# Kernel optimization log

Measured on AMD Instinct MI355X. Metric: run time of the kernel, lower is better.

## Reference

```python
import jax, jax.numpy as jnp
import numpy as np

D_MODEL = 1024
N_HEADS = 16
HEAD_DIM = D_MODEL // N_HEADS
SEQ_LEN = 2048
BATCH = 2
ROPE_THETA = 10000.0
EPS = 1e-8
SCALE = 1.0 / np.sqrt(HEAD_DIM)
MASK_VAL = -10000.0  # module uses -10000.0, not -inf


def _rope_tables(seq_len, head_dim, theta):
    inv = 1.0 / (theta ** (jnp.arange(0, head_dim, 2, dtype=jnp.float32) / head_dim))
    ang = jnp.arange(seq_len, dtype=jnp.float32)[:, None] * inv[None, :]  # [S, hd/2]
    return jnp.cos(ang), jnp.sin(ang)


def _apply_rope(t, cos, sin):
    # t: [B,S,H,hd]; pairs are consecutive elements (torch.view_as_complex layout)
    B, S, H, hd = t.shape
    tr = t.reshape(B, S, H, hd // 2, 2)
    te, to = tr[..., 0], tr[..., 1]
    c = cos[None, :, None, :]
    s = sin[None, :, None, :]
    out = jnp.stack([te * c - to * s, te * s + to * c], axis=-1)
    return out.reshape(B, S, H, hd)


def _rmsnorm(t, gamma):
    rms = jnp.sqrt(jnp.mean(t * t, axis=-1, keepdims=True) + EPS)
    return t / rms * gamma


def setup_inputs() -> dict:
    key = jax.random.key(0)
    ks = jax.random.split(key, 7)
    sw = 0.02  # weight scale ~ xavier
    return {
        "x": jax.random.normal(ks[0], (BATCH, SEQ_LEN, D_MODEL), jnp.float32),
        "wq": jax.random.normal(ks[1], (D_MODEL, D_MODEL), jnp.float32) * sw,
        "wk": jax.random.normal(ks[2], (D_MODEL, D_MODEL), jnp.float32) * sw,
        "wv": jax.random.normal(ks[3], (D_MODEL, D_MODEL), jnp.float32) * sw,
        "wo": jax.random.normal(ks[4], (D_MODEL, D_MODEL), jnp.float32) * sw,
        "q_gamma": jnp.ones((HEAD_DIM,), jnp.float32),
        "k_gamma": jnp.ones((HEAD_DIM,), jnp.float32),
    }


def reference(x, wq, wk, wv, wo, q_gamma, k_gamma):
    B, S, D = x.shape
    H, hd = N_HEADS, HEAD_DIM
    # projections (nn.Linear: y = x @ W.T)
    q = (x @ wq.T).reshape(B, S, H, hd)
    k = (x @ wk.T).reshape(B, S, H, hd)
    v = (x @ wv.T).reshape(B, S, H, hd)
    # RoPE
    cos, sin = _rope_tables(S, hd, ROPE_THETA)
    q = _apply_rope(q, cos, sin)
    k = _apply_rope(k, cos, sin)
    # QK RMSNorm
    q = _rmsnorm(q, q_gamma)
    k = _rmsnorm(k, k_gamma)
    # attention, causal mask with -10000.0 fill
    scores = jnp.einsum("bqhd,bkhd->bhqk", q, k) * SCALE
    causal = jnp.triu(jnp.ones((S, S), bool), k=1)
    scores = jnp.where(causal[None, None], MASK_VAL, scores)
    attn = jax.nn.softmax(scores, axis=-1)
    out = jnp.einsum("bhqk,bkhd->bqhd", attn, v).reshape(B, S, D)
    return out @ wo.T
```

## Files before the change

### kernel.cpp

```cpp
#include <hip/hip_runtime.h>
#include <hip/hip_bf16.h>
#include <stdint.h>

#define D_MODEL 1024
#define N_HEADS 16
#define HEAD_DIM 64
#define SEQ_LEN 2048
#define BATCH 2
#define M_TOK (BATCH * SEQ_LEN)
#define NQT (SEQ_LEN / 64)
#define SCL2 0.18033688011112042f
#define RMS_EPS 1e-8f

typedef __bf16 bf16x8 __attribute__((ext_vector_type(8)));
typedef float f32x4 __attribute__((ext_vector_type(4)));
typedef unsigned short us8 __attribute__((ext_vector_type(8)));
typedef unsigned short us4 __attribute__((ext_vector_type(4)));

__device__ __forceinline__ float bf2f(unsigned short u) {
    union { unsigned int i; float f; } x; x.i = ((unsigned int)u) << 16; return x.f;
}
__device__ __forceinline__ unsigned short f2bf(float f) {
    union { float f; unsigned int i; } x; x.f = f;
    unsigned int i = x.i;
    return (unsigned short)((i + 0x7FFFu + ((i >> 16) & 1u)) >> 16);
}
__device__ __forceinline__ f32x4 mfma16(bf16x8 a, bf16x8 b, f32x4 c) {
    return __builtin_amdgcn_mfma_f32_16x16x32_bf16(a, b, c, 0, 0, 0);
}

#define GLOAD16(gp, lp) __builtin_amdgcn_global_load_lds( \
    (__attribute__((address_space(1))) void*)(gp), \
    (__attribute__((address_space(3))) void*)(lp), 16, 0, 0)

__device__ __forceinline__ uint32_t lds_off(void* p) {
    return (uint32_t)(uintptr_t)(__attribute__((address_space(3))) char*)p;
}
__device__ __forceinline__ uint2 ds_tr16(uint32_t addr) {
    uint2 r;
    asm volatile("ds_read_b64_tr_b16 %0, %1" : "=v"(r) : "v"(addr));
    return r;
}

__global__ void f2bf_kernel(const float* __restrict__ in,
                            unsigned short* __restrict__ out, int n4) {
    int i = blockIdx.x * blockDim.x + threadIdx.x;
    if (i >= n4) return;
    float4 v = reinterpret_cast<const float4*>(in)[i];
    us4 o = { f2bf(v.x), f2bf(v.y), f2bf(v.z), f2bf(v.w) };
    reinterpret_cast<us4*>(out)[i] = o;
}

__global__ void f2bf_multi_kernel(const float* __restrict__ s0, const float* __restrict__ s1,
                                  const float* __restrict__ s2, const float* __restrict__ s3,
                                  unsigned short* __restrict__ d0, unsigned short* __restrict__ d1,
                                  unsigned short* __restrict__ d2, unsigned short* __restrict__ d3) {
    int i = blockIdx.x * 256 + threadIdx.x;
    int mm = i >> 18, j = i & 262143;
    const float* s = mm == 0 ? s0 : mm == 1 ? s1 : mm == 2 ? s2 : s3;
    unsigned short* d = mm == 0 ? d0 : mm == 1 ? d1 : mm == 2 ? d2 : d3;
    float4 v = reinterpret_cast<const float4*>(s)[j];
    us4 o = { f2bf(v.x), f2bf(v.y), f2bf(v.z), f2bf(v.w) };
    reinterpret_cast<us4*>(d)[j] = o;
}

__global__ void rope_tab_kernel(float2* __restrict__ tab) {
    int idx = blockIdx.x * 256 + threadIdx.x;
    int pos = idx >> 5, i = idx & 31;
    float inv = powf(10000.0f, -(float)(2 * i) / 64.0f);
    float ang = (float)pos * inv;
    tab[idx] = make_float2(cosf(ang), sinf(ang));
}

template <typename OutT, int NMAT>
__global__ __launch_bounds__(256, 2)
void gemm_bt_kernel(const unsigned short* __restrict__ A,
                    const unsigned short* __restrict__ B0,
                    const unsigned short* __restrict__ B1,
                    const unsigned short* __restrict__ B2,
                    OutT* __restrict__ C0, OutT* __restrict__ C1,
                    OutT* __restrict__ C2, int M, int N, int K) {
    __shared__ __align__(16) char lds[32768];
    char* Ab = lds;
    char* Bb = lds + 16384;

    const unsigned short* Bm = B0;
    OutT* Cm = C0;
    if (NMAT > 1) {
        int z = blockIdx.z;
        if (z == 1) { Bm = B1; Cm = C1; }
        else if (z == 2) { Bm = B2; Cm = C2; }
    }

    const int tid = threadIdx.x;
    const int w = tid >> 6, lane = tid & 63;
    const int g = lane >> 4, c15 = lane & 15;
    const int wr = w >> 1, wc = w & 1;
    const int m0 = blockIdx.y * 128, n0 = blockIdx.x * 128;
    const int row_s = tid >> 3, k8 = tid & 7;

    f32x4 acc[4][4] = {};
    const int NT = K >> 6;

    for (int kt = 0; kt < NT; ++kt) {
        const int kb = kt * 64;
        __syncthreads();
#pragma unroll
        for (int r = 0; r < 4; ++r) {
            int row = r * 32 + row_s;
            GLOAD16(A + (size_t)(m0 + row) * K + kb + k8 * 8, Ab + r * 4096 + w * 1024);
            GLOAD16(Bm + (size_t)(n0 + row) * K + kb + k8 * 8, Bb + r * 4096 + w * 1024);
        }
        __syncthreads();

        bf16x8 af[4][2], bfr[4][2];
#pragma unroll
        for (int mi = 0; mi < 4; ++mi)
#pragma unroll
            for (int kk = 0; kk < 2; ++kk) {
                af[mi][kk]  = *reinterpret_cast<const bf16x8*>(Ab + (wr * 64 + mi * 16 + c15) * 128 + kk * 64 + g * 16);
                bfr[mi][kk] = *reinterpret_cast<const bf16x8*>(Bb + (wc * 64 + mi * 16 + c15) * 128 + kk * 64 + g * 16);
            }
#pragma unroll
        for (int mi = 0; mi < 4; ++mi)
#pragma unroll
            for (int nj = 0; nj < 4; ++nj)
#pragma unroll
                for (int kk = 0; kk < 2; ++kk)
                    acc[mi][nj] = mfma16(af[mi][kk], bfr[nj][kk], acc[mi][nj]);
    }

#pragma unroll
    for (int mi = 0; mi < 4; ++mi)
#pragma unroll
        for (int nj = 0; nj < 4; ++nj)
#pragma unroll
            for (int r = 0; r < 4; ++r) {
                int row = m0 + wr * 64 + mi * 16 + g * 4 + r;
                int col = n0 + wc * 64 + nj * 16 + c15;
                float v = acc[mi][nj][r];
                if constexpr (sizeof(OutT) == 2)
                    Cm[(size_t)row * N + col] = f2bf(v);
                else
                    Cm[(size_t)row * N + col] = v;
            }
}

__global__ void rope_rms_kernel(unsigned short* __restrict__ Q,
                                unsigned short* __restrict__ Kt,
                                const float* __restrict__ qg,
                                const float* __restrict__ kg,
                                const float2* __restrict__ tab) {
    unsigned short* T = blockIdx.z ? Kt : Q;
    const float* gam = blockIdx.z ? kg : qg;
    int t = blockIdx.x * 256 + threadIdx.x;
    int rp = t >> 2, sub = t & 3;
    int s = (rp >> 4) & (SEQ_LEN - 1);
    unsigned short* p = T + (size_t)rp * 64 + sub * 16;
    float f[16];
    us8 v0 = *reinterpret_cast<const us8*>(p);
    us8 v1 = *reinterpret_cast<const us8*>(p + 8);
#pragma unroll
    for (int j = 0; j < 8; ++j) { f[j] = bf2f(v0[j]); f[8 + j] = bf2f(v1[j]); }
#pragma unroll
    for (int j = 0; j < 8; ++j) {
        float2 cs = tab[s * 32 + sub * 8 + j];
        float e = f[2 * j], o = f[2 * j + 1];
        f[2 * j]     = e * cs.x - o * cs.y;
        f[2 * j + 1] = e * cs.y + o * cs.x;
    }
    float ss = 0.f;
#pragma unroll
    for (int j = 0; j < 16; ++j) ss += f[j] * f[j];
    ss += __shfl_xor(ss, 1);
    ss += __shfl_xor(ss, 2);
    float rinv = rsqrtf(ss * (1.0f / 64.0f) + RMS_EPS);
    us8 o0, o1;
#pragma unroll
    for (int j = 0; j < 8; ++j) {
        o0[j] = f2bf(f[j] * rinv * gam[sub * 16 + j]);
        o1[j] = f2bf(f[8 + j] * rinv * gam[sub * 16 + 8 + j]);
    }
    *reinterpret_cast<us8*>(p) = o0;
    *reinterpret_cast<us8*>(p + 8) = o1;
}

__global__ __launch_bounds__(256, 2)
void attn_kernel(const unsigned short* __restrict__ Q,
                 const unsigned short* __restrict__ Kt,
                 const unsigned short* __restrict__ V,
                 unsigned short* __restrict__ O) {
    __shared__ __align__(16) char lds[40960];
    const int bh = blockIdx.y, b = bh >> 4, h = bh & 15;
    const int tid = threadIdx.x, w = tid >> 6, lane = tid & 63;
    const int g = lane >> 4, c15 = lane & 15;
    char* Pw = lds + 32768 + w * 2048;
    const size_t base_bh = (size_t)b * SEQ_LEN * D_MODEL + (size_t)h * HEAD_DIM;
    const int krow_s = tid >> 3, kcol_s = (tid & 7) * 16;
    const int psw = (c15 & 7) << 4;

    auto stageKV = [&](int buf, int kb) {
#pragma unroll
        for (int r = 0; r < 2; ++r) {
            int krow = r * 32 + krow_s;
            int cb = kcol_s ^ ((krow & 7) << 4);
            GLOAD16(Kt + base_bh + (size_t)(kb + krow) * D_MODEL + (cb >> 1),
                    lds + buf * 8192 + r * 4096 + w * 1024);
            int e = r * 2048 + tid * 8;
            int vk = ((e >> 8) << 2) + ((e >> 4) & 3);
            int vd = (((e >> 6) & 3) << 4) + (e & 15);
            GLOAD16(V + base_bh + (size_t)(kb + vk) * D_MODEL + vd,
                    lds + 16384 + buf * 8192 + r * 4096 + w * 1024);
        }
    };

#pragma unroll 1
    for (int half = 0; half < 2; ++half) {
        const int qt = half ? (NQT - 1 - blockIdx.x) : blockIdx.x;
        const int q0 = qt * 64, nt = qt + 1;
        const int q = q0 + w * 16 + c15;
        bf16x8 qf[2];
#pragma unroll
        for (int kk = 0; kk < 2; ++kk)
            qf[kk] = *reinterpret_cast<const bf16x8*>(Q + base_bh + (size_t)q * D_MODEL + kk * 32 + g * 8);
        f32x4 oacc[4] = {};
        float mrun = -1e30f, lrun = 0.f;

        stageKV(0, 0);
        __syncthreads();
        for (int it = 0; it < nt; ++it) {
            const int cur = it & 1, kb = it * 64;
            if (it + 1 < nt) stageKV(cur ^ 1, kb + 64);
            char* Kc = lds + cur * 8192;
            char* Vc = lds + 16384 + cur * 8192;

            f32x4 sacc[4] = {};
#pragma unroll
            for (int nj = 0; nj < 4; ++nj) {
                int kl = nj * 16 + c15, sw = (kl & 7) << 4;
#pragma unroll
                for (int kk = 0; kk < 2; ++kk) {
                    bf16x8 kf = *reinterpret_cast<const bf16x8*>(Kc + kl * 128 + ((kk * 64 + g * 16) ^ sw));
                    sacc[nj] = mfma16(kf, qf[kk], sacc[nj]);
                }
            }

            const bool diag = (it == nt - 1);
            float sv[4][4];
            float tmax = -1e30f;
#pragma unroll
            for (int nj = 0; nj < 4; ++nj)
#pragma unroll
                for (int r = 0; r < 4; ++r) {
                    float s = sacc[nj][r] * SCL2;
                    if (diag && (kb + nj * 16 + g * 4 + r > q)) s = -1e30f;
                    sv[nj][r] = s;
                    tmax = fmaxf(tmax, s);
                }
            tmax = fmaxf(tmax, __shfl_xor(tmax, 16));
            tmax = fmaxf(tmax, __shfl_xor(tmax, 32));
            float mnew = fmaxf(mrun, tmax);
            float alpha = exp2f(mrun - mnew);
            float rsum = 0.f;
#pragma unroll
            for (int nj = 0; nj < 4; ++nj) {
                us4 pw;
#pragma unroll
                for (int r = 0; r < 4; ++r) {
                    float p = exp2f(sv[nj][r] - mnew);
                    rsum += p;
                    pw[r] = f2bf(p);
                }
                *reinterpret_cast<us4*>(Pw + c15 * 128 + ((nj * 32 + g * 8) ^ psw)) = pw;
            }
            rsum += __shfl_xor(rsum, 16);
            rsum += __shfl_xor(rsum, 32);
            lrun = lrun * alpha + rsum;
            mrun = mnew;

            float ar[4];
#pragma unroll
            for (int r = 0; r < 4; ++r) ar[r] = __shfl(alpha, g * 4 + r, 16);
#pragma unroll
            for (int f = 0; f < 4; ++f)
#pragma unroll
                for (int r = 0; r < 4; ++r) oacc[f][r] *= ar[r];

            bf16x8 pf[2];
#pragma unroll
            for (int kk = 0; kk < 2; ++kk)
                pf[kk] = *reinterpret_cast<const bf16x8*>(Pw + c15 * 128 + ((kk * 64 + g * 16) ^ psw));
            uint32_t vbase = lds_off(Vc) + c15 * 8;
            uint2 vt[4][2][2];
#pragma unroll
            for (int f = 0; f < 4; ++f)
#pragma unroll
                for (int kk = 0; kk < 2; ++kk)
#pragma unroll
                    for (int hh = 0; hh < 2; ++hh)
                        vt[f][kk][hh] = ds_tr16(vbase + (uint32_t)((kk * 8 + g * 2 + hh) * 512 + f * 128));
            asm volatile("s_waitcnt lgkmcnt(0)" ::: "memory");
            __builtin_amdgcn_sched_barrier(0);
#pragma unroll
            for (int f = 0; f < 4; ++f)
#pragma unroll
                for (int kk = 0; kk < 2; ++kk) {
                    union { uint32_t u[4]; bf16x8 v; } fu;
                    fu.u[0] = vt[f][kk][0].x; fu.u[1] = vt[f][kk][0].y;
                    fu.u[2] = vt[f][kk][1].x; fu.u[3] = vt[f][kk][1].y;
                    oacc[f] = mfma16(pf[kk], fu.v, oacc[f]);
                }
            __syncthreads();
        }

        float li = 1.f / lrun;
        float lr[4];
#pragma unroll
        for (int r = 0; r < 4; ++r) lr[r] = __shfl(li, g * 4 + r, 16);
#pragma unroll
        for (int f = 0; f < 4; ++f)
#pragma unroll
            for (int r = 0; r < 4; ++r) {
                int qq = q0 + w * 16 + g * 4 + r;
                O[base_bh + (size_t)qq * D_MODEL + f * 16 + c15] = f2bf(oacc[f][r] * lr[r]);
            }
    }
}

extern "C" void kernel_launch(void* const* d_in, const int* in_sizes, int n_in,
                              void* d_out, int out_size, void* d_ws, size_t ws_size,
                              hipStream_t stream) {
    const float* x  = (const float*)d_in[0];
    const float* wq = (const float*)d_in[1];
    const float* wk = (const float*)d_in[2];
    const float* wv = (const float*)d_in[3];
    const float* wo = (const float*)d_in[4];
    const float* qg = (const float*)d_in[5];
    const float* kg = (const float*)d_in[6];
    float* out = (float*)d_out;

    char* ws = (char*)d_ws;
    const size_t MB = 1024ull * 1024ull;
    unsigned short* xb  = (unsigned short*)(ws);
    unsigned short* qb  = (unsigned short*)(ws + 8 * MB);
    unsigned short* kb  = (unsigned short*)(ws + 16 * MB);
    unsigned short* vb  = (unsigned short*)(ws + 24 * MB);
    unsigned short* ab  = (unsigned short*)(ws + 32 * MB);
    unsigned short* wqb = (unsigned short*)(ws + 40 * MB);
    unsigned short* wkb = (unsigned short*)(ws + 42 * MB);
    unsigned short* wvb = (unsigned short*)(ws + 44 * MB);
    unsigned short* wob = (unsigned short*)(ws + 46 * MB);
    float2* tab         = (float2*)(ws + 48 * MB);

    f2bf_kernel<<<4096, 256, 0, stream>>>(x, xb, M_TOK * D_MODEL / 4);
    f2bf_multi_kernel<<<4096, 256, 0, stream>>>(wq, wk, wv, wo, wqb, wkb, wvb, wob);
    rope_tab_kernel<<<256, 256, 0, stream>>>(tab);

    gemm_bt_kernel<unsigned short, 3><<<dim3(8, 32, 3), 256, 0, stream>>>(
        xb, wqb, wkb, wvb, qb, kb, vb, M_TOK, D_MODEL, D_MODEL);

    rope_rms_kernel<<<dim3(1024, 1, 2), 256, 0, stream>>>(qb, kb, qg, kg, tab);

    attn_kernel<<<dim3(16, 32), 256, 0, stream>>>(qb, kb, vb, ab);

    gemm_bt_kernel<float, 1><<<dim3(8, 32, 1), 256, 0, stream>>>(
        ab, wob, nullptr, nullptr, out, nullptr, nullptr, M_TOK, D_MODEL, D_MODEL);
}
```

Baseline: 215.0 us.

## Fuse prep kernels, fold RoPE+RMSNorm into QKV GEMM epilogue, defer softmax rescale

Merges the three conversion and RoPE-table kernels into one prep launch. RoPE and RMSNorm, including the softmax scale for Q, move into the QKV GEMM epilogue, which removes the separate read-modify-write pass over Q and K. The attention loop skips the running-max rescale unless the max rises by more than a threshold, packs bf16 with v_cvt_pk_bf16_f32, and raises wave priority around the MFMA blocks. The output projection uses 64-row tiles so more blocks run, and the epilogue adds shuffles and table loads inside the GEMM.

```diff
diff --git a/kernel.cpp b/kernel.cpp
--- a/kernel.cpp
+++ b/kernel.cpp
@@ -11,6 +11,7 @@
 #define NQT (SEQ_LEN / 64)
 #define SCL2 0.18033688011112042f
 #define RMS_EPS 1e-8f
+#define DEFER_THR 11.5f
 
 typedef __bf16 bf16x8 __attribute__((ext_vector_type(8)));
 typedef float f32x4 __attribute__((ext_vector_type(4)));
@@ -28,6 +29,11 @@
 __device__ __forceinline__ f32x4 mfma16(bf16x8 a, bf16x8 b, f32x4 c) {
     return __builtin_amdgcn_mfma_f32_16x16x32_bf16(a, b, c, 0, 0, 0);
 }
+__device__ __forceinline__ uint32_t cvtpk_bf16(float lo, float hi) {
+    uint32_t r;
+    asm("v_cvt_pk_bf16_f32 %0, %1, %2" : "=v"(r) : "v"(lo), "v"(hi));
+    return r;
+}
 
 #define GLOAD16(gp, lp) __builtin_amdgcn_global_load_lds( \
     (__attribute__((address_space(1))) void*)(gp), \
@@ -42,61 +48,61 @@
     return r;
 }
 
-__global__ void f2bf_kernel(const float* __restrict__ in,
-                            unsigned short* __restrict__ out, int n4) {
-    int i = blockIdx.x * blockDim.x + threadIdx.x;
-    if (i >= n4) return;
-    float4 v = reinterpret_cast<const float4*>(in)[i];
-    us4 o = { f2bf(v.x), f2bf(v.y), f2bf(v.z), f2bf(v.w) };
-    reinterpret_cast<us4*>(out)[i] = o;
-}
-
-__global__ void f2bf_multi_kernel(const float* __restrict__ s0, const float* __restrict__ s1,
-                                  const float* __restrict__ s2, const float* __restrict__ s3,
-                                  unsigned short* __restrict__ d0, unsigned short* __restrict__ d1,
-                                  unsigned short* __restrict__ d2, unsigned short* __restrict__ d3) {
-    int i = blockIdx.x * 256 + threadIdx.x;
-    int mm = i >> 18, j = i & 262143;
-    const float* s = mm == 0 ? s0 : mm == 1 ? s1 : mm == 2 ? s2 : s3;
-    unsigned short* d = mm == 0 ? d0 : mm == 1 ? d1 : mm == 2 ? d2 : d3;
-    float4 v = reinterpret_cast<const float4*>(s)[j];
-    us4 o = { f2bf(v.x), f2bf(v.y), f2bf(v.z), f2bf(v.w) };
-    reinterpret_cast<us4*>(d)[j] = o;
-}
-
-__global__ void rope_tab_kernel(float2* __restrict__ tab) {
-    int idx = blockIdx.x * 256 + threadIdx.x;
-    int pos = idx >> 5, i = idx & 31;
-    float inv = powf(10000.0f, -(float)(2 * i) / 64.0f);
-    float ang = (float)pos * inv;
-    tab[idx] = make_float2(cosf(ang), sinf(ang));
-}
-
-template <typename OutT, int NMAT>
+__global__ void prep_kernel(const float* __restrict__ x,  const float* __restrict__ wq,
+                            const float* __restrict__ wk, const float* __restrict__ wv,
+                            const float* __restrict__ wo,
+                            unsigned short* __restrict__ xb,  unsigned short* __restrict__ wqb,
+                            unsigned short* __restrict__ wkb, unsigned short* __restrict__ wvb,
+                            unsigned short* __restrict__ wob, float2* __restrict__ tab2) {
+    int bid = blockIdx.x;
+    if (bid < 8192) {
+        int i = bid * 256 + threadIdx.x;
+        const float* s; unsigned short* d; int j;
+        if (i < 1048576) { s = x; d = xb; j = i; }
+        else {
+            int t = i - 1048576; int mm = t >> 18; j = t & 262143;
+            s = mm == 0 ? wq : mm == 1 ? wk : mm == 2 ? wv : wo;
+            d = mm == 0 ? wqb : mm == 1 ? wkb : mm == 2 ? wvb : wob;
+        }
+        float4 v = reinterpret_cast<const float4*>(s)[j];
+        us4 o = { f2bf(v.x), f2bf(v.y), f2bf(v.z), f2bf(v.w) };
+        reinterpret_cast<us4*>(d)[j] = o;
+    } else {
+        int idx = (bid - 8192) * 256 + threadIdx.x;
+        int i = idx >> 11, sp = idx & 2047;
+        float inv = powf(10000.0f, -(float)(2 * i) / 64.0f);
+        float ang = (float)sp * inv;
+        tab2[idx] = make_float2(cosf(ang), sinf(ang));
+    }
+}
+
 __global__ __launch_bounds__(256, 2)
-void gemm_bt_kernel(const unsigned short* __restrict__ A,
-                    const unsigned short* __restrict__ B0,
-                    const unsigned short* __restrict__ B1,
-                    const unsigned short* __restrict__ B2,
-                    OutT* __restrict__ C0, OutT* __restrict__ C1,
-                    OutT* __restrict__ C2, int M, int N, int K) {
+void gemm_qkv_kernel(const unsigned short* __restrict__ A,
+                     const unsigned short* __restrict__ Bq,
+                     const unsigned short* __restrict__ Bk,
+                     const unsigned short* __restrict__ Bv,
+                     unsigned short* __restrict__ Cq,
+                     unsigned short* __restrict__ Ck,
+                     unsigned short* __restrict__ Cv,
+                     const float* __restrict__ qg,
+                     const float* __restrict__ kg,
+                     const float2* __restrict__ tab2) {
+    const int K = D_MODEL, N = D_MODEL;
     __shared__ __align__(16) char lds[32768];
     char* Ab = lds;
     char* Bb = lds + 16384;
 
-    const unsigned short* Bm = B0;
-    OutT* Cm = C0;
-    if (NMAT > 1) {
-        int z = blockIdx.z;
-        if (z == 1) { Bm = B1; Cm = C1; }
-        else if (z == 2) { Bm = B2; Cm = C2; }
-    }
+    const int nb = blockIdx.x;
+    const int mtype = nb >> 3;
+    const int ncol = (nb & 7) * 128;
+    const unsigned short* Bm = mtype == 0 ? Bq : mtype == 1 ? Bk : Bv;
+    unsigned short* Cm = mtype == 0 ? Cq : mtype == 1 ? Ck : Cv;
 
     const int tid = threadIdx.x;
     const int w = tid >> 6, lane = tid & 63;
     const int g = lane >> 4, c15 = lane & 15;
     const int wr = w >> 1, wc = w & 1;
-    const int m0 = blockIdx.y * 128, n0 = blockIdx.x * 128;
+    const int m0 = blockIdx.y * 128;
     const int row_s = tid >> 3, k8 = tid & 7;
 
     f32x4 acc[4][4] = {};
@@ -109,7 +115,7 @@
         for (int r = 0; r < 4; ++r) {
             int row = r * 32 + row_s;
             GLOAD16(A + (size_t)(m0 + row) * K + kb + k8 * 8, Ab + r * 4096 + w * 1024);
-            GLOAD16(Bm + (size_t)(n0 + row) * K + kb + k8 * 8, Bb + r * 4096 + w * 1024);
+            GLOAD16(Bm + (size_t)(ncol + row) * K + kb + k8 * 8, Bb + r * 4096 + w * 1024);
         }
         __syncthreads();
 
@@ -130,59 +136,131 @@
                     acc[mi][nj] = mfma16(af[mi][kk], bfr[nj][kk], acc[mi][nj]);
     }
 
-#pragma unroll
-    for (int mi = 0; mi < 4; ++mi)
+    if (mtype == 2) {
+#pragma unroll
+        for (int mi = 0; mi < 4; ++mi)
+#pragma unroll
+            for (int nj = 0; nj < 4; ++nj)
+#pragma unroll
+                for (int r = 0; r < 4; ++r) {
+                    int row = m0 + wr * 64 + mi * 16 + g * 4 + r;
+                    int col = ncol + wc * 64 + nj * 16 + c15;
+                    Cm[(size_t)row * N + col] = f2bf(acc[mi][nj][r]);
+                }
+        return;
+    }
+
+    const float* gam = mtype ? kg : qg;
+    const float qsc = mtype ? 1.0f : SCL2;
+    float g4[4];
+#pragma unroll
+    for (int nj = 0; nj < 4; ++nj) g4[nj] = gam[nj * 16 + c15] * qsc;
+    const int ihalf = c15 >> 1;
+
+#pragma unroll
+    for (int mi = 0; mi < 4; ++mi) {
+        int rbase = m0 + wr * 64 + mi * 16 + g * 4;
+        int srow = rbase & (SEQ_LEN - 1);
+        float2 cs[4][4];
+#pragma unroll
+        for (int nj = 0; nj < 4; ++nj) {
+            const float4* tp = reinterpret_cast<const float4*>(tab2 + (size_t)(nj * 8 + ihalf) * SEQ_LEN + srow);
+            float4 lo = tp[0], hi = tp[1];
+            cs[nj][0] = make_float2(lo.x, lo.y); cs[nj][1] = make_float2(lo.z, lo.w);
+            cs[nj][2] = make_float2(hi.x, hi.y); cs[nj][3] = make_float2(hi.z, hi.w);
+        }
+        float rot[4][4];
 #pragma unroll
         for (int nj = 0; nj < 4; ++nj)
 #pragma unroll
             for (int r = 0; r < 4; ++r) {
-                int row = m0 + wr * 64 + mi * 16 + g * 4 + r;
+                float v = acc[mi][nj][r];
+                float pv = __shfl_xor(v, 1);
+                float c = cs[nj][r].x, s = cs[nj][r].y;
+                rot[nj][r] = (c15 & 1) ? fmaf(pv, s, v * c) : fmaf(-pv, s, v * c);
+            }
+#pragma unroll
+        for (int r = 0; r < 4; ++r) {
+            float ss = rot[0][r] * rot[0][r] + rot[1][r] * rot[1][r]
+                     + rot[2][r] * rot[2][r] + rot[3][r] * rot[3][r];
+            ss += __shfl_xor(ss, 1);
+            ss += __shfl_xor(ss, 2);
+            ss += __shfl_xor(ss, 4);
+            ss += __shfl_xor(ss, 8);
+            float rinv = rsqrtf(ss * (1.0f / 64.0f) + RMS_EPS);
+#pragma unroll
+            for (int nj = 0; nj < 4; ++nj) {
+                int col = ncol + wc * 64 + nj * 16 + c15;
+                Cm[(size_t)(rbase + r) * N + col] = f2bf(rot[nj][r] * rinv * g4[nj]);
+            }
+        }
+    }
+}
+
+__global__ __launch_bounds__(256, 2)
+void gemm_proj_kernel(const unsigned short* __restrict__ A,
+                      const unsigned short* __restrict__ B,
+                      float* __restrict__ C) {
+    const int K = D_MODEL, N = D_MODEL;
+    __shared__ __align__(16) char lds[24576];
+    char* Ab = lds;
+    char* Bb = lds + 8192;
+
+    const int tid = threadIdx.x;
+    const int w = tid >> 6, lane = tid & 63;
+    const int g = lane >> 4, c15 = lane & 15;
+    const int wr = w >> 1, wc = w & 1;
+    const int m0 = blockIdx.y * 64, n0 = blockIdx.x * 128;
+    const int row_s = tid >> 3, k8 = tid & 7;
+
+    f32x4 acc[2][4] = {};
+    const int NT = K >> 6;
+
+    for (int kt = 0; kt < NT; ++kt) {
+        const int kb = kt * 64;
+        __syncthreads();
+#pragma unroll
+        for (int r = 0; r < 2; ++r) {
+            int row = r * 32 + row_s;
+            GLOAD16(A + (size_t)(m0 + row) * K + kb + k8 * 8, Ab + r * 4096 + w * 1024);
+        }
+#pragma unroll
+        for (int r = 0; r < 4; ++r) {
+            int row = r * 32 + row_s;
+            GLOAD16(B + (size_t)(n0 + row) * K + kb + k8 * 8, Bb + r * 4096 + w * 1024);
+        }
+        __syncthreads();
+
+        bf16x8 af[2][2], bfr[4][2];
+#pragma unroll
+        for (int mi = 0; mi < 2; ++mi)
+#pragma unroll
+            for (int kk = 0; kk < 2; ++kk)
+                af[mi][kk] = *reinterpret_cast<const bf16x8*>(Ab + (wr * 32 + mi * 16 + c15) * 128 + kk * 64 + g * 16);
+#pragma unroll
+        for (int nj = 0; nj < 4; ++nj)
+#pragma unroll
+            for (int kk = 0; kk < 2; ++kk)
+                bfr[nj][kk] = *reinterpret_cast<const bf16x8*>(Bb + (wc * 64 + nj * 16 + c15) * 128 + kk * 64 + g * 16);
+#pragma unroll
+        for (int mi = 0; mi < 2; ++mi)
+#pragma unroll
+            for (int nj = 0; nj < 4; ++nj)
+#pragma unroll
+                for (int kk = 0; kk < 2; ++kk)
+                    acc[mi][nj] = mfma16(af[mi][kk], bfr[nj][kk], acc[mi][nj]);
+    }
+
+#pragma unroll
+    for (int mi = 0; mi < 2; ++mi)
+#pragma unroll
+        for (int nj = 0; nj < 4; ++nj)
+#pragma unroll
+            for (int r = 0; r < 4; ++r) {
+                int row = m0 + wr * 32 + mi * 16 + g * 4 + r;
                 int col = n0 + wc * 64 + nj * 16 + c15;
-                float v = acc[mi][nj][r];
-                if constexpr (sizeof(OutT) == 2)
-                    Cm[(size_t)row * N + col] = f2bf(v);
-                else
-                    Cm[(size_t)row * N + col] = v;
-            }
-}
-
-__global__ void rope_rms_kernel(unsigned short* __restrict__ Q,
-                                unsigned short* __restrict__ Kt,
-                                const float* __restrict__ qg,
-                                const float* __restrict__ kg,
-                                const float2* __restrict__ tab) {
-    unsigned short* T = blockIdx.z ? Kt : Q;
-    const float* gam = blockIdx.z ? kg : qg;
-    int t = blockIdx.x * 256 + threadIdx.x;
-    int rp = t >> 2, sub = t & 3;
-    int s = (rp >> 4) & (SEQ_LEN - 1);
-    unsigned short* p = T + (size_t)rp * 64 + sub * 16;
-    float f[16];
-    us8 v0 = *reinterpret_cast<const us8*>(p);
-    us8 v1 = *reinterpret_cast<const us8*>(p + 8);
-#pragma unroll
-    for (int j = 0; j < 8; ++j) { f[j] = bf2f(v0[j]); f[8 + j] = bf2f(v1[j]); }
-#pragma unroll
-    for (int j = 0; j < 8; ++j) {
-        float2 cs = tab[s * 32 + sub * 8 + j];
-        float e = f[2 * j], o = f[2 * j + 1];
-        f[2 * j]     = e * cs.x - o * cs.y;
-        f[2 * j + 1] = e * cs.y + o * cs.x;
-    }
-    float ss = 0.f;
-#pragma unroll
-    for (int j = 0; j < 16; ++j) ss += f[j] * f[j];
-    ss += __shfl_xor(ss, 1);
-    ss += __shfl_xor(ss, 2);
-    float rinv = rsqrtf(ss * (1.0f / 64.0f) + RMS_EPS);
-    us8 o0, o1;
-#pragma unroll
-    for (int j = 0; j < 8; ++j) {
-        o0[j] = f2bf(f[j] * rinv * gam[sub * 16 + j]);
-        o1[j] = f2bf(f[8 + j] * rinv * gam[sub * 16 + 8 + j]);
-    }
-    *reinterpret_cast<us8*>(p) = o0;
-    *reinterpret_cast<us8*>(p + 8) = o1;
+                C[(size_t)row * N + col] = acc[mi][nj][r];
+            }
 }
 
 __global__ __launch_bounds__(256, 2)
@@ -235,6 +313,7 @@
             char* Vc = lds + 16384 + cur * 8192;
 
             f32x4 sacc[4] = {};
+            __builtin_amdgcn_s_setprio(1);
 #pragma unroll
             for (int nj = 0; nj < 4; ++nj) {
                 int kl = nj * 16 + c15, sw = (kl & 7) << 4;
@@ -244,6 +323,7 @@
                     sacc[nj] = mfma16(kf, qf[kk], sacc[nj]);
                 }
             }
+            __builtin_amdgcn_s_setprio(0);
 
             const bool diag = (it == nt - 1);
             float sv[4][4];
@@ -252,39 +332,42 @@
             for (int nj = 0; nj < 4; ++nj)
 #pragma unroll
                 for (int r = 0; r < 4; ++r) {
-                    float s = sacc[nj][r] * SCL2;
+                    float s = sacc[nj][r];
                     if (diag && (kb + nj * 16 + g * 4 + r > q)) s = -1e30f;
                     sv[nj][r] = s;
                     tmax = fmaxf(tmax, s);
                 }
             tmax = fmaxf(tmax, __shfl_xor(tmax, 16));
             tmax = fmaxf(tmax, __shfl_xor(tmax, 32));
-            float mnew = fmaxf(mrun, tmax);
-            float alpha = exp2f(mrun - mnew);
+
+            float alpha = 1.0f;
+            if (__any(tmax > mrun + DEFER_THR)) {
+                float mnew = fmaxf(mrun, tmax);
+                alpha = exp2f(mrun - mnew);
+                mrun = mnew;
+                float ar[4];
+#pragma unroll
+                for (int r = 0; r < 4; ++r) ar[r] = __shfl(alpha, g * 4 + r, 16);
+#pragma unroll
+                for (int f = 0; f < 4; ++f)
+#pragma unroll
+                    for (int r = 0; r < 4; ++r) oacc[f][r] *= ar[r];
+            }
+
             float rsum = 0.f;
 #pragma unroll
             for (int nj = 0; nj < 4; ++nj) {
-                us4 pw;
-#pragma unroll
-                for (int r = 0; r < 4; ++r) {
-                    float p = exp2f(sv[nj][r] - mnew);
-                    rsum += p;
-                    pw[r] = f2bf(p);
-                }
-                *reinterpret_cast<us4*>(Pw + c15 * 128 + ((nj * 32 + g * 8) ^ psw)) = pw;
+                float p0 = exp2f(sv[nj][0] - mrun);
+                float p1 = exp2f(sv[nj][1] - mrun);
+                float p2 = exp2f(sv[nj][2] - mrun);
+                float p3 = exp2f(sv[nj][3] - mrun);
+                rsum += (p0 + p1) + (p2 + p3);
+                uint2 pw = { cvtpk_bf16(p0, p1), cvtpk_bf16(p2, p3) };
+                *reinterpret_cast<uint2*>(Pw + c15 * 128 + ((nj * 32 + g * 8) ^ psw)) = pw;
             }
             rsum += __shfl_xor(rsum, 16);
             rsum += __shfl_xor(rsum, 32);
             lrun = lrun * alpha + rsum;
-            mrun = mnew;
-
-            float ar[4];
-#pragma unroll
-            for (int r = 0; r < 4; ++r) ar[r] = __shfl(alpha, g * 4 + r, 16);
-#pragma unroll
-            for (int f = 0; f < 4; ++f)
-#pragma unroll
-                for (int r = 0; r < 4; ++r) oacc[f][r] *= ar[r];
 
             bf16x8 pf[2];
 #pragma unroll
@@ -301,6 +384,7 @@
                         vt[f][kk][hh] = ds_tr16(vbase + (uint32_t)((kk * 8 + g * 2 + hh) * 512 + f * 128));
             asm volatile("s_waitcnt lgkmcnt(0)" ::: "memory");
             __builtin_amdgcn_sched_barrier(0);
+            __builtin_amdgcn_s_setprio(1);
 #pragma unroll
             for (int f = 0; f < 4; ++f)
 #pragma unroll
@@ -310,6 +394,7 @@
                     fu.u[2] = vt[f][kk][1].x; fu.u[3] = vt[f][kk][1].y;
                     oacc[f] = mfma16(pf[kk], fu.v, oacc[f]);
                 }
+            __builtin_amdgcn_s_setprio(0);
             __syncthreads();
         }
 
@@ -350,19 +435,14 @@
     unsigned short* wkb = (unsigned short*)(ws + 42 * MB);
     unsigned short* wvb = (unsigned short*)(ws + 44 * MB);
     unsigned short* wob = (unsigned short*)(ws + 46 * MB);
-    float2* tab         = (float2*)(ws + 48 * MB);
-
-    f2bf_kernel<<<4096, 256, 0, stream>>>(x, xb, M_TOK * D_MODEL / 4);
-    f2bf_multi_kernel<<<4096, 256, 0, stream>>>(wq, wk, wv, wo, wqb, wkb, wvb, wob);
-    rope_tab_kernel<<<256, 256, 0, stream>>>(tab);
-
-    gemm_bt_kernel<unsigned short, 3><<<dim3(8, 32, 3), 256, 0, stream>>>(
-        xb, wqb, wkb, wvb, qb, kb, vb, M_TOK, D_MODEL, D_MODEL);
-
-    rope_rms_kernel<<<dim3(1024, 1, 2), 256, 0, stream>>>(qb, kb, qg, kg, tab);
+    float2* tab2        = (float2*)(ws + 48 * MB);
+
+    prep_kernel<<<8448, 256, 0, stream>>>(x, wq, wk, wv, wo, xb, wqb, wkb, wvb, wob, tab2);
+
+    gemm_qkv_kernel<<<dim3(24, 32), 256, 0, stream>>>(
+        xb, wqb, wkb, wvb, qb, kb, vb, qg, kg, tab2);
 
     attn_kernel<<<dim3(16, 32), 256, 0, stream>>>(qb, kb, vb, ab);
 
-    gemm_bt_kernel<float, 1><<<dim3(8, 32, 1), 256, 0, stream>>>(
-        ab, wob, nullptr, nullptr, out, nullptr, nullptr, M_TOK, D_MODEL, D_MODEL);
-}
+    gemm_proj_kernel<<<dim3(8, 64), 256, 0, stream>>>(ab, wob, out);
+}
```

New measurement: 196.6 us. -8.6%, faster.
